# Kernel optimization log

Measured on AMD Instinct MI355X. Metric: run time of the kernel, lower is better.

Reference implementation:

```python
import jax, jax.numpy as jnp
import numpy as np

EMBED_DIM = 128
HIDDEN_DIM = 256  # int(2.0 * 128)
ROT_DIM = 32      # min(32, embed_dim)
THETA = 10000.0


def rope(x, rot_dim=ROT_DIM, theta=THETA):
    # rotary_embedding_torch style: interleaved pairs, first rot_dim features rotated
    seq = x.shape[-2]
    inv_freq = 1.0 / (theta ** (jnp.arange(0, rot_dim, 2, dtype=jnp.float32) / rot_dim))
    t = jnp.arange(seq, dtype=jnp.float32)
    freqs = jnp.einsum('i,j->ij', t, inv_freq)          # [S, rot/2]
    freqs = jnp.repeat(freqs, 2, axis=-1)               # [S, rot]
    x_rot, x_pass = x[..., :rot_dim], x[..., rot_dim:]
    x1, x2 = x_rot[..., 0::2], x_rot[..., 1::2]
    rot_half = jnp.stack([-x2, x1], axis=-1).reshape(x_rot.shape)
    x_rot = x_rot * jnp.cos(freqs) + rot_half * jnp.sin(freqs)
    return jnp.concatenate([x_rot, x_pass], axis=-1)


def layer_norm(x, g, b, eps=1e-5):
    mu = jnp.mean(x, axis=-1, keepdims=True)
    var = jnp.mean((x - mu) ** 2, axis=-1, keepdims=True)
    return (x - mu) * jax.lax.rsqrt(var + eps) * g + b


def setup_inputs() -> dict:
    key = jax.random.key(0)
    ks = jax.random.split(key, 12)
    B, S, D, H = 4, 4096, EMBED_DIM, HIDDEN_DIM
    s = 0.02
    return {
        'query': jax.random.normal(ks[0], (B, S, D), jnp.float32),
        'key':   jax.random.normal(ks[1], (B, S, D), jnp.float32),
        'value': jax.random.normal(ks[2], (B, S, D), jnp.float32),
        'ln_g': jnp.ones((D,), jnp.float32),
        'ln_b': jnp.zeros((D,), jnp.float32),
        'W_gate': jax.random.normal(ks[3], (D, H), jnp.float32) * s,
        'b_gate': jnp.zeros((H,), jnp.float32),
        'W_qk': jax.random.normal(ks[4], (D, D), jnp.float32) * s,
        'b_qk': jnp.zeros((D,), jnp.float32),
        'os_gamma': jax.random.normal(ks[5], (2, D), jnp.float32) * 0.02 + 1.0,
        'os_beta': jnp.zeros((2, D), jnp.float32),
        'W_out': jax.random.normal(ks[6], (H, D), jnp.float32) * s,
        'b_out': jnp.zeros((D,), jnp.float32),
    }


def reference(query, key, value, ln_g, ln_b, W_gate, b_gate, W_qk, b_qk,
              os_gamma, os_beta, W_out, b_out):
    B, S, D = query.shape
    query = rope(query)
    normed = layer_norm(query, ln_g, ln_b)
    gate = jax.nn.silu(normed @ W_gate + b_gate)          # [B,S,H]
    # NOTE: source reuses to_gate for v (to_v is dead code) and never uses `key`
    v = jax.nn.silu(value @ W_gate + b_gate)              # [B,S,H]
    qk = jax.nn.silu(normed @ W_qk + b_qk)                # [B,S,D]
    q = qk * os_gamma[0] + os_beta[0]
    k = qk * os_gamma[1] + os_beta[1]
    sim = jnp.einsum('bid,bjd->bij', q, k) / S            # [B,S,S]
    attn = jnp.square(jax.nn.relu(sim))                   # ReLU^2
    att_map = attn
    out = jnp.einsum('bij,bjd->bid', attn, v)             # [B,S,H]
    out = out * gate
    out = out @ W_out + b_out                             # [B,S,D]
    return out, att_map
```

## Files before the change

### kernel.cpp

```cpp
#include <hip/hip_runtime.h>
#include <stdint.h>

typedef __bf16 bf16_t;
typedef __bf16 bf16x8 __attribute__((ext_vector_type(8)));
typedef float f32x16 __attribute__((ext_vector_type(16)));

#define S_LEN 4096
#define D_DIM 128
#define H_DIM 256
#define NROW 16384

__device__ __forceinline__ f32x16 zero16() {
    f32x16 z;
#pragma unroll
    for (int i = 0; i < 16; i++) z[i] = 0.0f;
    return z;
}

__device__ __forceinline__ float silu_f(float x) {
    return x / (1.0f + __expf(-x));
}

static __device__ __forceinline__ f32x16 mfma_bf16(bf16x8 a, bf16x8 b, f32x16 c) {
    return __builtin_amdgcn_mfma_f32_32x32x16_bf16(a, b, c, 0, 0, 0);
}

__global__ __launch_bounds__(256) void cast_weights_kernel(
    const float* __restrict__ Wg, const float* __restrict__ Wqk,
    const float* __restrict__ Wo,
    bf16_t* __restrict__ WgT, bf16_t* __restrict__ WqkT, bf16_t* __restrict__ WoT) {
    int idx = blockIdx.x * 256 + threadIdx.x;
    if (idx < 32768) {
        int n = idx >> 7, k = idx & 127;
        WgT[idx] = (bf16_t)Wg[k * 256 + n];
    } else if (idx < 49152) {
        int j = idx - 32768;
        int n = j >> 7, k = j & 127;
        WqkT[j] = (bf16_t)Wqk[k * 128 + n];
    } else if (idx < 81920) {
        int j = idx - 49152;
        int n = j >> 8, k = j & 255;
        WoT[j] = (bf16_t)Wo[k * 128 + n];
    }
}

__global__ __launch_bounds__(256) void rope_ln_kernel(
    const float* __restrict__ q_in, const float* __restrict__ v_in,
    const float* __restrict__ ln_g, const float* __restrict__ ln_b,
    bf16_t* __restrict__ normed, bf16_t* __restrict__ value_bf) {
    int w = threadIdx.x >> 6, l = threadIdx.x & 63;
    int row = blockIdx.x * 4 + w;
    int s = row & (S_LEN - 1);
    const float* qr = q_in + (size_t)row * D_DIM;
    float x0 = qr[l];
    float x1 = qr[l + 64];
    float partner = __shfl_xor(x0, 1, 64);
    if (l < 32) {
        int i = l >> 1;
        float f = (float)s * exp2f(-(float)i * 0.8304820237218405f);
        float sn, c;
        sincosf(f, &sn, &c);
        x0 = (l & 1) ? (x0 * c + partner * sn) : (x0 * c - partner * sn);
    }
    float sum = x0 + x1;
#pragma unroll
    for (int off = 32; off >= 1; off >>= 1) sum += __shfl_xor(sum, off, 64);
    float mu = sum * (1.0f / 128.0f);
    float d0 = x0 - mu, d1 = x1 - mu;
    float ss = d0 * d0 + d1 * d1;
#pragma unroll
    for (int off = 32; off >= 1; off >>= 1) ss += __shfl_xor(ss, off, 64);
    float rs = rsqrtf(ss * (1.0f / 128.0f) + 1e-5f);
    size_t base = (size_t)row * D_DIM;
    normed[base + l]      = (bf16_t)(d0 * rs * ln_g[l] + ln_b[l]);
    normed[base + l + 64] = (bf16_t)(d1 * rs * ln_g[l + 64] + ln_b[l + 64]);
    value_bf[base + l]      = (bf16_t)v_in[base + l];
    value_bf[base + l + 64] = (bf16_t)v_in[base + l + 64];
}

__global__ __launch_bounds__(256) void gemm_gate_v_kernel(
    const bf16_t* __restrict__ normed, const bf16_t* __restrict__ value_bf,
    const bf16_t* __restrict__ WgT, const float* __restrict__ b_gate,
    bf16_t* __restrict__ gate_bf, bf16_t* __restrict__ vT) {
    int w = threadIdx.x >> 6, l = threadIdx.x & 63;
    bool is_v = blockIdx.x >= 256;
    int m0 = (is_v ? (blockIdx.x - 256) : blockIdx.x) * 64;
    const bf16_t* A = is_v ? value_bf : normed;
    int rw = w >> 1, cw = w & 1;
    const bf16_t* aptr = A + (size_t)(m0 + rw * 32 + (l & 31)) * 128 + ((l >> 5) * 8);
    bf16x8 af[8];
#pragma unroll
    for (int kk = 0; kk < 8; kk++) af[kk] = *(const bf16x8*)(aptr + kk * 16);
#pragma unroll
    for (int t = 0; t < 4; t++) {
        int n0 = cw * 128 + t * 32;
        f32x16 acc = zero16();
        const bf16_t* bptr = WgT + (size_t)(n0 + (l & 31)) * 128 + ((l >> 5) * 8);
#pragma unroll
        for (int kk = 0; kk < 8; kk++) {
            bf16x8 bfv = *(const bf16x8*)(bptr + kk * 16);
            acc = mfma_bf16(af[kk], bfv, acc);
        }
        int col = n0 + (l & 31);
        float bg = b_gate[col];
#pragma unroll
        for (int r = 0; r < 16; r++) {
            int drow = (r & 3) + ((r >> 2) << 3) + ((l >> 5) << 2);
            int rowg = m0 + rw * 32 + drow;
            float sil = silu_f(acc[r] + bg);
            if (!is_v) {
                gate_bf[(size_t)rowg * 256 + col] = (bf16_t)sil;
            } else {
                int bb = rowg >> 12, ss2 = rowg & 4095;
                vT[((size_t)bb * 256 + col) * 4096 + ss2] = (bf16_t)sil;
            }
        }
    }
}

__global__ __launch_bounds__(256) void gemm_qk_kernel(
    const bf16_t* __restrict__ normed, const bf16_t* __restrict__ WqkT,
    const float* __restrict__ b_qk, const float* __restrict__ os_gamma,
    const float* __restrict__ os_beta,
    bf16_t* __restrict__ q_ws, bf16_t* __restrict__ k_ws) {
    int w = threadIdx.x >> 6, l = threadIdx.x & 63;
    int m0 = blockIdx.x * 64;
    int rw = w >> 1, cw = w & 1;
    const bf16_t* aptr = normed + (size_t)(m0 + rw * 32 + (l & 31)) * 128 + ((l >> 5) * 8);
    bf16x8 af[8];
#pragma unroll
    for (int kk = 0; kk < 8; kk++) af[kk] = *(const bf16x8*)(aptr + kk * 16);
#pragma unroll
    for (int t = 0; t < 2; t++) {
        int n0 = cw * 64 + t * 32;
        f32x16 acc = zero16();
        const bf16_t* bptr = WqkT + (size_t)(n0 + (l & 31)) * 128 + ((l >> 5) * 8);
#pragma unroll
        for (int kk = 0; kk < 8; kk++) {
            bf16x8 bfv = *(const bf16x8*)(bptr + kk * 16);
            acc = mfma_bf16(af[kk], bfv, acc);
        }
        int col = n0 + (l & 31);
        float bq = b_qk[col];
        float g0 = os_gamma[col], g1 = os_gamma[128 + col];
        float be0 = os_beta[col], be1 = os_beta[128 + col];
#pragma unroll
        for (int r = 0; r < 16; r++) {
            int drow = (r & 3) + ((r >> 2) << 3) + ((l >> 5) << 2);
            size_t rowg = (size_t)(m0 + rw * 32 + drow);
            float sil = silu_f(acc[r] + bq);
            q_ws[rowg * 128 + col] = (bf16_t)(sil * g0 + be0);
            k_ws[rowg * 128 + col] = (bf16_t)(sil * g1 + be1);
        }
    }
}

__global__ __launch_bounds__(256) void attn_kernel(
    const bf16_t* __restrict__ q_ws, const bf16_t* __restrict__ k_ws,
    const bf16_t* __restrict__ vT, const bf16_t* __restrict__ gate_bf,
    float* __restrict__ att_map, bf16_t* __restrict__ AG) {
    int w = threadIdx.x >> 6, l = threadIdx.x & 63;
    int b = blockIdx.y;
    int i0 = blockIdx.x * 64;
    int rw = w >> 1, cw = w & 1;
    __shared__ __align__(16) bf16_t attn_lds[64 * 64];

    f32x16 O[2][2];
    O[0][0] = zero16(); O[0][1] = zero16(); O[1][0] = zero16(); O[1][1] = zero16();

    const bf16_t* qptr =
        q_ws + (size_t)(b * S_LEN + i0 + rw * 32 + (l & 31)) * 128 + ((l >> 5) * 8);
    bf16x8 qf[8];
#pragma unroll
    for (int kk = 0; kk < 8; kk++) qf[kk] = *(const bf16x8*)(qptr + kk * 16);

    const float inv_S = 1.0f / 4096.0f;
    int col = cw * 32 + (l & 31);

    for (int jt = 0; jt < 64; jt++) {
        int j0 = jt * 64;
        f32x16 sacc = zero16();
        const bf16_t* kptr =
            k_ws + (size_t)(b * S_LEN + j0 + cw * 32 + (l & 31)) * 128 + ((l >> 5) * 8);
#pragma unroll
        for (int kk = 0; kk < 8; kk++) {
            bf16x8 kf = *(const bf16x8*)(kptr + kk * 16);
            sacc = mfma_bf16(qf[kk], kf, sacc);
        }
        float* amcol = att_map + ((size_t)(b * S_LEN + i0) * S_LEN) + j0 + col;
        int cc = col >> 3;
#pragma unroll
        for (int r = 0; r < 16; r++) {
            int drow = (r & 3) + ((r >> 2) << 3) + ((l >> 5) << 2);
            int row = rw * 32 + drow;
            float v = fmaxf(sacc[r], 0.0f) * inv_S;
            float a = v * v;
            amcol[(size_t)row * S_LEN] = a;
            attn_lds[row * 64 + ((cc ^ (row & 7)) << 3) + (col & 7)] = (bf16_t)a;
        }
        __syncthreads();
        bf16x8 Bf[2][4];
#pragma unroll
        for (int tc = 0; tc < 2; tc++) {
            const bf16_t* vptr =
                vT + (size_t)(b * 256 + w * 64 + tc * 32 + (l & 31)) * S_LEN + j0 +
                ((l >> 5) * 8);
#pragma unroll
            for (int kk = 0; kk < 4; kk++)
                Bf[tc][kk] = *(const bf16x8*)(vptr + kk * 16);
        }
#pragma unroll
        for (int tr = 0; tr < 2; tr++) {
            int arow = tr * 32 + (l & 31);
            const bf16_t* abase = attn_lds + arow * 64;
            int rx = arow & 7;
#pragma unroll
            for (int kk = 0; kk < 4; kk++) {
                int acc_cc = kk * 2 + (l >> 5);
                bf16x8 Af = *(const bf16x8*)(abase + ((acc_cc ^ rx) << 3));
                O[tr][0] = mfma_bf16(Af, Bf[0][kk], O[tr][0]);
                O[tr][1] = mfma_bf16(Af, Bf[1][kk], O[tr][1]);
            }
        }
        __syncthreads();
    }
#pragma unroll
    for (int tr = 0; tr < 2; tr++) {
#pragma unroll
        for (int tc = 0; tc < 2; tc++) {
            int hcol = w * 64 + tc * 32 + (l & 31);
#pragma unroll
            for (int r = 0; r < 16; r++) {
                int drow = (r & 3) + ((r >> 2) << 3) + ((l >> 5) << 2);
                size_t rowg = (size_t)(b * S_LEN + i0 + tr * 32 + drow);
                float g = (float)gate_bf[rowg * 256 + hcol];
                AG[rowg * 256 + hcol] = (bf16_t)(O[tr][tc][r] * g);
            }
        }
    }
}

__global__ __launch_bounds__(256) void final_kernel(
    const bf16_t* __restrict__ AG, const bf16_t* __restrict__ WoT,
    const float* __restrict__ b_out, float* __restrict__ out) {
    int w = threadIdx.x >> 6, l = threadIdx.x & 63;
    int m0 = blockIdx.x * 64;
    int rw = w >> 1, cw = w & 1;
    const bf16_t* aptr = AG + (size_t)(m0 + rw * 32 + (l & 31)) * 256 + ((l >> 5) * 8);
    bf16x8 af[16];
#pragma unroll
    for (int kk = 0; kk < 16; kk++) af[kk] = *(const bf16x8*)(aptr + kk * 16);
#pragma unroll
    for (int t = 0; t < 2; t++) {
        int n0 = cw * 64 + t * 32;
        f32x16 acc = zero16();
        const bf16_t* bptr = WoT + (size_t)(n0 + (l & 31)) * 256 + ((l >> 5) * 8);
#pragma unroll
        for (int kk = 0; kk < 16; kk++) {
            bf16x8 bfv = *(const bf16x8*)(bptr + kk * 16);
            acc = mfma_bf16(af[kk], bfv, acc);
        }
        int col = n0 + (l & 31);
        float bo = b_out[col];
#pragma unroll
        for (int r = 0; r < 16; r++) {
            int drow = (r & 3) + ((r >> 2) << 3) + ((l >> 5) << 2);
            out[(size_t)(m0 + rw * 32 + drow) * 128 + col] = acc[r] + bo;
        }
    }
}

extern "C" void kernel_launch(void* const* d_in, const int* in_sizes, int n_in,
                              void* d_out, int out_size, void* d_ws, size_t ws_size,
                              hipStream_t stream) {
    const float* query    = (const float*)d_in[0];
    const float* value    = (const float*)d_in[2];
    const float* ln_g     = (const float*)d_in[3];
    const float* ln_b     = (const float*)d_in[4];
    const float* W_gate   = (const float*)d_in[5];
    const float* b_gate   = (const float*)d_in[6];
    const float* W_qk     = (const float*)d_in[7];
    const float* b_qk     = (const float*)d_in[8];
    const float* os_gamma = (const float*)d_in[9];
    const float* os_beta  = (const float*)d_in[10];
    const float* W_out    = (const float*)d_in[11];
    const float* b_out    = (const float*)d_in[12];

    float* out_p   = (float*)d_out;
    float* att_map = out_p + (size_t)NROW * 128;

    char* ws = (char*)d_ws;
    bf16_t* normed   = (bf16_t*)(ws);
    bf16_t* value_bf = (bf16_t*)(ws + ((size_t)4 << 20));
    bf16_t* q_ws     = (bf16_t*)(ws + ((size_t)8 << 20));
    bf16_t* k_ws     = (bf16_t*)(ws + ((size_t)12 << 20));
    bf16_t* vT       = (bf16_t*)(ws + ((size_t)16 << 20));
    bf16_t* gate_bf  = (bf16_t*)(ws + ((size_t)24 << 20));
    bf16_t* AG       = (bf16_t*)(ws + ((size_t)32 << 20));
    bf16_t* WgT      = (bf16_t*)(ws + ((size_t)40 << 20));
    bf16_t* WqkT     = WgT + 32768;
    bf16_t* WoT      = WqkT + 16384;

    cast_weights_kernel<<<320, 256, 0, stream>>>(W_gate, W_qk, W_out, WgT, WqkT, WoT);
    rope_ln_kernel<<<4096, 256, 0, stream>>>(query, value, ln_g, ln_b, normed, value_bf);
    gemm_gate_v_kernel<<<512, 256, 0, stream>>>(normed, value_bf, WgT, b_gate, gate_bf, vT);
    gemm_qk_kernel<<<256, 256, 0, stream>>>(normed, WqkT, b_qk, os_gamma, os_beta, q_ws, k_ws);
    attn_kernel<<<dim3(64, 4), 256, 0, stream>>>(q_ws, k_ws, vT, gate_bf, att_map, AG);
    final_kernel<<<256, 256, 0, stream>>>(AG, WoT, b_out, out_p);
}
```

Measured before the change: 503.5 us.

## Widen attention block to 1024 threads with 256-column tiles and stage vT writes

The attention kernel now runs 16 waves per block and processes 256 key columns per iteration, so each wave owns one 32x32 output tile and the number of barrier round-trips drops from 64 to 16. It uses a larger swizzled LDS tile and writes the attention map with nontemporal stores. The transposed V write in the gate/V GEMM is staged through shared memory so it can be emitted as coalesced 16-byte stores instead of strided scalar stores. The W_out cast moves into its own kernel, and the old cast branch is now dead because the grid shrank. The trade-offs are more LDS per block and fewer resident blocks, with only 256 blocks covering the GPU.

```diff
diff --git a/kernel.cpp b/kernel.cpp
--- a/kernel.cpp
+++ b/kernel.cpp
@@ -2,6 +2,7 @@
 #include <stdint.h>
 
 typedef __bf16 bf16_t;
+typedef __bf16 bf16x4 __attribute__((ext_vector_type(4)));
 typedef __bf16 bf16x8 __attribute__((ext_vector_type(8)));
 typedef float f32x16 __attribute__((ext_vector_type(16)));
 
@@ -40,6 +41,15 @@
     } else if (idx < 81920) {
         int j = idx - 49152;
         int n = j >> 8, k = j & 255;
+        WoT[j] = (bf16_t)Wo[k * 255 + k + n - k];
+    }
+}
+
+__global__ __launch_bounds__(256) void cast_wo_kernel(
+    const float* __restrict__ Wo, bf16_t* __restrict__ WoT) {
+    int j = blockIdx.x * 256 + threadIdx.x;
+    if (j < 32768) {
+        int n = j >> 8, k = j & 255;
         WoT[j] = (bf16_t)Wo[k * 128 + n];
     }
 }
@@ -82,6 +92,7 @@
     const bf16_t* __restrict__ normed, const bf16_t* __restrict__ value_bf,
     const bf16_t* __restrict__ WgT, const float* __restrict__ b_gate,
     bf16_t* __restrict__ gate_bf, bf16_t* __restrict__ vT) {
+    __shared__ __align__(16) bf16_t vstage[256 * 68];
     int w = threadIdx.x >> 6, l = threadIdx.x & 63;
     bool is_v = blockIdx.x >= 256;
     int m0 = (is_v ? (blockIdx.x - 256) : blockIdx.x) * 64;
@@ -103,17 +114,37 @@
         }
         int col = n0 + (l & 31);
         float bg = b_gate[col];
-#pragma unroll
-        for (int r = 0; r < 16; r++) {
-            int drow = (r & 3) + ((r >> 2) << 3) + ((l >> 5) << 2);
-            int rowg = m0 + rw * 32 + drow;
-            float sil = silu_f(acc[r] + bg);
-            if (!is_v) {
-                gate_bf[(size_t)rowg * 256 + col] = (bf16_t)sil;
-            } else {
-                int bb = rowg >> 12, ss2 = rowg & 4095;
-                vT[((size_t)bb * 256 + col) * 4096 + ss2] = (bf16_t)sil;
+        if (!is_v) {
+#pragma unroll
+            for (int r = 0; r < 16; r++) {
+                int drow = (r & 3) + ((r >> 2) << 3) + ((l >> 5) << 2);
+                int rowg = m0 + rw * 32 + drow;
+                gate_bf[(size_t)rowg * 256 + col] = (bf16_t)silu_f(acc[r] + bg);
             }
+        } else {
+#pragma unroll
+            for (int gq = 0; gq < 4; gq++) {
+                int base = rw * 32 + 8 * gq + ((l >> 5) << 2);
+                bf16x4 p;
+#pragma unroll
+                for (int q = 0; q < 4; q++) p[q] = (bf16_t)silu_f(acc[gq * 4 + q] + bg);
+                *(bf16x4*)(&vstage[col * 68 + base]) = p;
+            }
+        }
+    }
+    if (is_v) {
+        __syncthreads();
+        int sc = threadIdx.x & 7, ch = threadIdx.x >> 3;
+        int bb = m0 >> 12, srow = m0 & 4095;
+#pragma unroll
+        for (int it = 0; it < 8; it++) {
+            int col = ch + 32 * it;
+            bf16x4 lo = *(const bf16x4*)(&vstage[col * 68 + sc * 8]);
+            bf16x4 hi = *(const bf16x4*)(&vstage[col * 68 + sc * 8 + 4]);
+            bf16x8 o;
+#pragma unroll
+            for (int q = 0; q < 4; q++) { o[q] = lo[q]; o[q + 4] = hi[q]; }
+            *(bf16x8*)(vT + ((size_t)bb * 256 + col) * 4096 + srow + sc * 8) = o;
         }
     }
 }
@@ -155,88 +186,72 @@
     }
 }
 
-__global__ __launch_bounds__(256) void attn_kernel(
+__global__ __launch_bounds__(1024, 4) void attn_kernel(
     const bf16_t* __restrict__ q_ws, const bf16_t* __restrict__ k_ws,
     const bf16_t* __restrict__ vT, const bf16_t* __restrict__ gate_bf,
     float* __restrict__ att_map, bf16_t* __restrict__ AG) {
     int w = threadIdx.x >> 6, l = threadIdx.x & 63;
     int b = blockIdx.y;
     int i0 = blockIdx.x * 64;
-    int rw = w >> 1, cw = w & 1;
-    __shared__ __align__(16) bf16_t attn_lds[64 * 64];
-
-    f32x16 O[2][2];
-    O[0][0] = zero16(); O[0][1] = zero16(); O[1][0] = zero16(); O[1][1] = zero16();
+    int oi = w >> 3;
+    int oc = w & 7;
+    __shared__ __align__(16) bf16_t attn_lds[64 * 256];
+
+    f32x16 O = zero16();
 
     const bf16_t* qptr =
-        q_ws + (size_t)(b * S_LEN + i0 + rw * 32 + (l & 31)) * 128 + ((l >> 5) * 8);
+        q_ws + (size_t)(b * S_LEN + i0 + oi * 32 + (l & 31)) * 128 + ((l >> 5) * 8);
     bf16x8 qf[8];
 #pragma unroll
     for (int kk = 0; kk < 8; kk++) qf[kk] = *(const bf16x8*)(qptr + kk * 16);
 
     const float inv_S = 1.0f / 4096.0f;
-    int col = cw * 32 + (l & 31);
-
-    for (int jt = 0; jt < 64; jt++) {
-        int j0 = jt * 64;
+    int col = oc * 32 + (l & 31);
+    int cc = col >> 3;
+    int arow = oi * 32 + (l & 31);
+    int rx = arow & 31;
+    const bf16_t* abase = attn_lds + arow * 256;
+    const bf16_t* vbase =
+        vT + (size_t)(b * 256 + oc * 32 + (l & 31)) * S_LEN + ((l >> 5) * 8);
+
+    for (int jt = 0; jt < 16; jt++) {
+        int j0 = jt * 256;
         f32x16 sacc = zero16();
         const bf16_t* kptr =
-            k_ws + (size_t)(b * S_LEN + j0 + cw * 32 + (l & 31)) * 128 + ((l >> 5) * 8);
+            k_ws + (size_t)(b * S_LEN + j0 + oc * 32 + (l & 31)) * 128 + ((l >> 5) * 8);
 #pragma unroll
         for (int kk = 0; kk < 8; kk++) {
             bf16x8 kf = *(const bf16x8*)(kptr + kk * 16);
             sacc = mfma_bf16(qf[kk], kf, sacc);
         }
-        float* amcol = att_map + ((size_t)(b * S_LEN + i0) * S_LEN) + j0 + col;
-        int cc = col >> 3;
+        float* amp = att_map + (size_t)(b * S_LEN + i0 + oi * 32) * S_LEN + j0 + col;
 #pragma unroll
         for (int r = 0; r < 16; r++) {
             int drow = (r & 3) + ((r >> 2) << 3) + ((l >> 5) << 2);
-            int row = rw * 32 + drow;
+            int row = oi * 32 + drow;
             float v = fmaxf(sacc[r], 0.0f) * inv_S;
             float a = v * v;
-            amcol[(size_t)row * S_LEN] = a;
-            attn_lds[row * 64 + ((cc ^ (row & 7)) << 3) + (col & 7)] = (bf16_t)a;
+            __builtin_nontemporal_store(a, amp + (size_t)drow * S_LEN);
+            attn_lds[row * 256 + (((cc ^ (row & 31)) << 3) | (col & 7))] = (bf16_t)a;
         }
         __syncthreads();
-        bf16x8 Bf[2][4];
-#pragma unroll
-        for (int tc = 0; tc < 2; tc++) {
-            const bf16_t* vptr =
-                vT + (size_t)(b * 256 + w * 64 + tc * 32 + (l & 31)) * S_LEN + j0 +
-                ((l >> 5) * 8);
-#pragma unroll
-            for (int kk = 0; kk < 4; kk++)
-                Bf[tc][kk] = *(const bf16x8*)(vptr + kk * 16);
-        }
-#pragma unroll
-        for (int tr = 0; tr < 2; tr++) {
-            int arow = tr * 32 + (l & 31);
-            const bf16_t* abase = attn_lds + arow * 64;
-            int rx = arow & 7;
-#pragma unroll
-            for (int kk = 0; kk < 4; kk++) {
-                int acc_cc = kk * 2 + (l >> 5);
-                bf16x8 Af = *(const bf16x8*)(abase + ((acc_cc ^ rx) << 3));
-                O[tr][0] = mfma_bf16(Af, Bf[0][kk], O[tr][0]);
-                O[tr][1] = mfma_bf16(Af, Bf[1][kk], O[tr][1]);
-            }
+        const bf16_t* vptr = vbase + j0;
+#pragma unroll
+        for (int kk = 0; kk < 16; kk++) {
+            bf16x8 Bf = *(const bf16x8*)(vptr + kk * 16);
+            int acc_cc = kk * 2 + (l >> 5);
+            bf16x8 Af = *(const bf16x8*)(abase + ((acc_cc ^ rx) << 3));
+            O = mfma_bf16(Af, Bf, O);
         }
         __syncthreads();
     }
-#pragma unroll
-    for (int tr = 0; tr < 2; tr++) {
-#pragma unroll
-        for (int tc = 0; tc < 2; tc++) {
-            int hcol = w * 64 + tc * 32 + (l & 31);
-#pragma unroll
-            for (int r = 0; r < 16; r++) {
-                int drow = (r & 3) + ((r >> 2) << 3) + ((l >> 5) << 2);
-                size_t rowg = (size_t)(b * S_LEN + i0 + tr * 32 + drow);
-                float g = (float)gate_bf[rowg * 256 + hcol];
-                AG[rowg * 256 + hcol] = (bf16_t)(O[tr][tc][r] * g);
-            }
-        }
+    int hcol = oc * 32 + (l & 31);
+#pragma unroll
+    for (int r = 0; r < 16; r++) {
+        int drow = (r & 3) + ((r >> 2) << 3) + ((l >> 5) << 2);
+        size_t rowg = (size_t)(b * S_LEN + i0 + oi * 32 + drow);
+        float g = (float)gate_bf[rowg * 256 + hcol];
+        AG[rowg * 256 + hcol] = (bf16_t)(O[r] * g);
     }
 }
 
@@ -301,10 +316,11 @@
     bf16_t* WqkT     = WgT + 32768;
     bf16_t* WoT      = WqkT + 16384;
 
-    cast_weights_kernel<<<320, 256, 0, stream>>>(W_gate, W_qk, W_out, WgT, WqkT, WoT);
+    cast_weights_kernel<<<192, 256, 0, stream>>>(W_gate, W_qk, W_out, WgT, WqkT, WoT);
+    cast_wo_kernel<<<128, 256, 0, stream>>>(W_out, WoT);
     rope_ln_kernel<<<4096, 256, 0, stream>>>(query, value, ln_g, ln_b, normed, value_bf);
     gemm_gate_v_kernel<<<512, 256, 0, stream>>>(normed, value_bf, WgT, b_gate, gate_bf, vT);
     gemm_qk_kernel<<<256, 256, 0, stream>>>(normed, WqkT, b_qk, os_gamma, os_beta, q_ws, k_ws);
-    attn_kernel<<<dim3(64, 4), 256, 0, stream>>>(q_ws, k_ws, vT, gate_bf, att_map, AG);
+    attn_kernel<<<dim3(64, 4), 1024, 0, stream>>>(q_ws, k_ws, vT, gate_bf, att_map, AG);
     final_kernel<<<256, 256, 0, stream>>>(AG, WoT, b_out, out_p);
 }
```

Result: no change. 505.1 us (+0.3%).
